# Kernel tuning notes

Measured on AMD Instinct MI355X. Metric: run time of the kernel, lower is better.

The kernel has to match this reference:

```python
import jax, jax.numpy as jnp
import numpy as np

N, E, C, H = 100000, 1600000, 64, 8
D = C // H  # head_dim = 8
LN_EPS = 1e-5


def _layer_norm(x, g, b):
    m = jnp.mean(x, axis=-1, keepdims=True)
    v = jnp.mean((x - m) ** 2, axis=-1, keepdims=True)
    return (x - m) * jax.lax.rsqrt(v + LN_EPS) * g + b


def setup_inputs() -> dict:
    key = jax.random.key(0)
    ks = jax.random.split(key, 20)
    s = 1.0 / np.sqrt(C)

    def lin(k, din, dout):
        return jax.random.uniform(k, (din, dout), jnp.float32, -1.0, 1.0) / np.sqrt(din)

    inp = {
        "node_states": jax.random.normal(ks[0], (N, C), jnp.float32),
        "edge_states": jax.random.normal(ks[1], (E, C), jnp.float32),
        "edge_index": jax.random.randint(ks[2], (2, E), 0, N),
        # attention projections
        "wq": lin(ks[3], C, C), "bq": jnp.zeros((C,), jnp.float32),
        "wk": lin(ks[4], C, C), "bk": jnp.zeros((C,), jnp.float32),
        "wv": lin(ks[5], C, C), "bv": jnp.zeros((C,), jnp.float32),
        "we": lin(ks[6], C, C), "be": jnp.zeros((C,), jnp.float32),
        "wno": lin(ks[7], C, C), "bno": jnp.zeros((C,), jnp.float32),
        "weo": lin(ks[8], H, C), "beo": jnp.zeros((C,), jnp.float32),
        # layer norms
        "n1g": jnp.ones((C,), jnp.float32), "n1b": jnp.zeros((C,), jnp.float32),
        "e1g": jnp.ones((C,), jnp.float32), "e1b": jnp.zeros((C,), jnp.float32),
        "n2g": jnp.ones((C,), jnp.float32), "n2b": jnp.zeros((C,), jnp.float32),
        "e2g": jnp.ones((C,), jnp.float32), "e2b": jnp.zeros((C,), jnp.float32),
        # node FFN
        "nf1w": lin(ks[9], C, 2 * C), "nf1b": jnp.zeros((2 * C,), jnp.float32),
        "nf2w": lin(ks[10], 2 * C, C), "nf2b": jnp.zeros((C,), jnp.float32),
        # edge FFN
        "ef1w": lin(ks[11], C, 2 * C), "ef1b": jnp.zeros((2 * C,), jnp.float32),
        "ef2w": lin(ks[12], 2 * C, C), "ef2b": jnp.zeros((C,), jnp.float32),
    }
    return inp


def reference(node_states, edge_states, wq, bq, wk, bk, wv, bv, we, be,
              wno, bno, weo, beo, n1g, n1b, e1g, e1b, n2g, n2b, e2g, e2b,
              nf1w, nf1b, nf2w, nf2b, ef1w, ef1b, ef2w, ef2b, edge_index):
    n = node_states.shape[0]
    e = edge_states.shape[0]
    src, dst = edge_index[0], edge_index[1]

    # pre-norm inputs
    ni = _layer_norm(node_states, n1g, n1b)
    ei = _layer_norm(edge_states, e1g, e1b)

    # projections -> [N,H,D] / [E,H,D]
    q = (ni @ wq + bq).reshape(n, H, D)
    k = (ni @ wk + bk).reshape(n, H, D)
    v = (ni @ wv + bv).reshape(n, H, D)
    edge_heads = ei.reshape(e, H, D)
    edge_score_heads = (ei @ we + be).reshape(e, H, D)

    # per-edge scores [E,H]
    scores = ((q[src] * k[dst]).sum(-1) + (edge_score_heads * edge_heads).sum(-1)) / np.sqrt(D)

    # segment softmax over edges sharing the same source node (per head)
    seg_max = jax.ops.segment_max(scores, src, num_segments=n)
    exp_s = jnp.exp(scores - seg_max[src])
    denom = jax.ops.segment_sum(exp_s, src, num_segments=n)
    attention = exp_s / (denom[src] + 1e-12)  # [E,H]

    # weighted scatter-add aggregation
    neighbor_state = ni[dst].reshape(e, H, D)
    weighted = attention[:, :, None] * (v[dst] * neighbor_state)  # [E,H,D]
    aggregated = jax.ops.segment_sum(weighted, src, num_segments=n).reshape(n, C)

    node_update = aggregated @ wno + bno
    edge_update = attention @ weo + beo

    node_s = node_states + node_update
    edge_s = edge_states + edge_update

    # FFN blocks with pre-norm residuals
    node_s = node_s + (jax.nn.relu(_layer_norm(node_s, n2g, n2b) @ nf1w + nf1b) @ nf2w + nf2b)
    edge_s = edge_s + (jax.nn.relu(_layer_norm(edge_s, e2g, e2b) @ ef1w + ef1b) @ ef2w + ef2b)
    return node_s, edge_s, attention
```

## Files before the change

### kernel.cpp

```cpp
#include <hip/hip_runtime.h>
#include <math.h>

#define NN 100000
#define EE 1600000

__device__ __forceinline__ float wsum64(float x){
  #pragma unroll
  for (int o = 32; o; o >>= 1) x += __shfl_xor(x, o, 64);
  return x;
}

__global__ __launch_bounds__(256) void k_node_pre(
    const float* __restrict__ ns,
    const float* __restrict__ wq, const float* __restrict__ bq,
    const float* __restrict__ wk, const float* __restrict__ bk,
    const float* __restrict__ wv, const float* __restrict__ bv,
    const float* __restrict__ n1g, const float* __restrict__ n1b,
    float* __restrict__ ni, float* __restrict__ q,
    float* __restrict__ k, float* __restrict__ v)
{
  __shared__ float swq[4096], swk[4096], swv[4096];
  for (int i = threadIdx.x; i < 4096; i += 256){ swq[i]=wq[i]; swk[i]=wk[i]; swv[i]=wv[i]; }
  __syncthreads();
  const int wave = threadIdx.x >> 6, lane = threadIdx.x & 63;
  const float gq = bq[lane], gk = bk[lane], gv = bv[lane];
  const float g1 = n1g[lane], b1 = n1b[lane];
  for (int n = blockIdx.x*4 + wave; n < NN; n += gridDim.x*4){
    const float x = ns[(size_t)n*64 + lane];
    const float m = wsum64(x) * (1.f/64.f);
    const float d = x - m;
    const float var = wsum64(d*d) * (1.f/64.f);
    const float niv = d * rsqrtf(var + 1e-5f) * g1 + b1;
    ni[(size_t)n*64 + lane] = niv;
    float aq = gq, ak = gk, av = gv;
    #pragma unroll
    for (int i = 0; i < 64; i++){
      const float e_ = __shfl(niv, i, 64);
      aq = fmaf(e_, swq[i*64 + lane], aq);
      ak = fmaf(e_, swk[i*64 + lane], ak);
      av = fmaf(e_, swv[i*64 + lane], av);
    }
    q[(size_t)n*64 + lane] = aq;
    k[(size_t)n*64 + lane] = ak;
    v[(size_t)n*64 + lane] = av;
  }
}

__global__ __launch_bounds__(256) void k_edge1(
    const float* __restrict__ es_in, const int* __restrict__ eidx,
    const float* __restrict__ we, const float* __restrict__ be,
    const float* __restrict__ e1g, const float* __restrict__ e1b,
    const float* __restrict__ q, const float* __restrict__ k,
    float* __restrict__ expo, float* __restrict__ denom)
{
  __shared__ float swe[4096];
  for (int i = threadIdx.x; i < 4096; i += 256) swe[i] = we[i];
  __syncthreads();
  const int wave = threadIdx.x >> 6, lane = threadIdx.x & 63;
  const float gbe = be[lane], g1 = e1g[lane], b1 = e1b[lane];
  for (size_t e = (size_t)blockIdx.x*4 + wave; e < EE; e += (size_t)gridDim.x*4){
    const float x = es_in[e*64 + lane];
    const float m = wsum64(x) * (1.f/64.f);
    const float d = x - m;
    const float var = wsum64(d*d) * (1.f/64.f);
    const float ei = d * rsqrtf(var + 1e-5f) * g1 + b1;
    float es = gbe;
    #pragma unroll
    for (int i = 0; i < 64; i++){
      es = fmaf(__shfl(ei, i, 64), swe[i*64 + lane], es);
    }
    const int src = eidx[e], dst = eidx[(size_t)EE + e];
    const float qs = q[(size_t)src*64 + lane];
    const float kd = k[(size_t)dst*64 + lane];
    float p = fmaf(qs, kd, es*ei);
    p += __shfl_xor(p, 1, 64); p += __shfl_xor(p, 2, 64); p += __shfl_xor(p, 4, 64);
    const float ev = __expf(p * 0.35355339059327373f);
    const float hv = __shfl(ev, (lane & 7)*8, 64);
    if (lane < 8){
      expo[e*8 + lane] = hv;
      atomicAdd(&denom[(size_t)src*8 + lane], hv);
    }
  }
}

__global__ __launch_bounds__(512) void k_edge2(
    const float* __restrict__ es_in, const int* __restrict__ eidx,
    const float* __restrict__ ni, const float* __restrict__ v,
    const float* __restrict__ weo, const float* __restrict__ beo,
    const float* __restrict__ e2g, const float* __restrict__ e2b,
    const float* __restrict__ ef1w, const float* __restrict__ ef1b,
    const float* __restrict__ ef2w, const float* __restrict__ ef2b,
    float* __restrict__ att, const float* __restrict__ denom,
    float* __restrict__ agg, float* __restrict__ eout)
{
  __shared__ float sf1[8192];
  __shared__ float sf2[8192];
  for (int i = threadIdx.x; i < 8192; i += 512){ sf1[i] = ef1w[i]; sf2[i] = ef2w[i]; }
  __syncthreads();
  const int wave = threadIdx.x >> 6, lane = threadIdx.x & 63;
  const int h = lane >> 3;
  float wo[8];
  #pragma unroll
  for (int hh = 0; hh < 8; hh++) wo[hh] = weo[hh*64 + lane];
  const float gbeo = beo[lane], g2 = e2g[lane], b2 = e2b[lane];
  const float gb1a = ef1b[lane], gb1b = ef1b[64 + lane], gb2 = ef2b[lane];

  for (size_t e = (size_t)blockIdx.x*8 + wave; e < EE; e += (size_t)gridDim.x*8){
    const int src = eidx[e], dst = eidx[(size_t)EE + e];
    const float ev  = att[e*8 + h];
    const float den = denom[(size_t)src*8 + h];
    const float a   = ev / (den + 1e-12f);
    const float av_ = __shfl(a, (lane & 7)*8, 64);
    if (lane < 8) att[e*8 + lane] = av_;

    const float vd = v[(size_t)dst*64 + lane];
    const float nd = ni[(size_t)dst*64 + lane];
    atomicAdd(&agg[(size_t)src*64 + lane], a*vd*nd);

    float eu = gbeo;
    #pragma unroll
    for (int hh = 0; hh < 8; hh++)
      eu = fmaf(__shfl(a, hh*8, 64), wo[hh], eu);
    const float esv = es_in[e*64 + lane] + eu;

    const float m = wsum64(esv) * (1.f/64.f);
    const float d = esv - m;
    const float var = wsum64(d*d) * (1.f/64.f);
    const float t = d * rsqrtf(var + 1e-5f) * g2 + b2;

    float h1a = gb1a, h1b = gb1b;
    #pragma unroll
    for (int i = 0; i < 64; i++){
      const float ti = __shfl(t, i, 64);
      h1a = fmaf(ti, sf1[i*128 + lane],      h1a);
      h1b = fmaf(ti, sf1[i*128 + 64 + lane], h1b);
    }
    h1a = fmaxf(h1a, 0.f); h1b = fmaxf(h1b, 0.f);
    float o = gb2;
    #pragma unroll
    for (int j = 0; j < 64; j++){
      o = fmaf(__shfl(h1a, j, 64), sf2[j*64 + lane],        o);
      o = fmaf(__shfl(h1b, j, 64), sf2[(64 + j)*64 + lane], o);
    }
    eout[e*64 + lane] = esv + o;
  }
}

__global__ __launch_bounds__(256) void k_node2(
    const float* __restrict__ ns, const float* __restrict__ agg,
    const float* __restrict__ wno, const float* __restrict__ bno,
    float* __restrict__ nout)
{
  __shared__ float sw[4096];
  for (int i = threadIdx.x; i < 4096; i += 256) sw[i] = wno[i];
  __syncthreads();
  const int wave = threadIdx.x >> 6, lane = threadIdx.x & 63;
  const float gb = bno[lane];
  for (int n = blockIdx.x*4 + wave; n < NN; n += gridDim.x*4){
    const float ag = agg[(size_t)n*64 + lane];
    float acc = gb;
    #pragma unroll
    for (int i = 0; i < 64; i++)
      acc = fmaf(__shfl(ag, i, 64), sw[i*64 + lane], acc);
    nout[(size_t)n*64 + lane] = ns[(size_t)n*64 + lane] + acc;
  }
}

__global__ __launch_bounds__(256) void k_node_ffn(
    float* __restrict__ x_inout,
    const float* __restrict__ g, const float* __restrict__ b,
    const float* __restrict__ f1w, const float* __restrict__ f1b,
    const float* __restrict__ f2w, const float* __restrict__ f2b)
{
  __shared__ float sf1[8192], sf2[8192];
  for (int i = threadIdx.x; i < 8192; i += 256){ sf1[i] = f1w[i]; sf2[i] = f2w[i]; }
  __syncthreads();
  const int wave = threadIdx.x >> 6, lane = threadIdx.x & 63;
  const float gg = g[lane], gb = b[lane];
  const float b1a = f1b[lane], b1b = f1b[64 + lane], bb2 = f2b[lane];
  for (int n = blockIdx.x*4 + wave; n < NN; n += gridDim.x*4){
    const float x = x_inout[(size_t)n*64 + lane];
    const float m = wsum64(x) * (1.f/64.f);
    const float d = x - m;
    const float var = wsum64(d*d) * (1.f/64.f);
    const float t = d * rsqrtf(var + 1e-5f) * gg + gb;
    float h1a = b1a, h1b = b1b;
    #pragma unroll
    for (int i = 0; i < 64; i++){
      const float ti = __shfl(t, i, 64);
      h1a = fmaf(ti, sf1[i*128 + lane],      h1a);
      h1b = fmaf(ti, sf1[i*128 + 64 + lane], h1b);
    }
    h1a = fmaxf(h1a, 0.f); h1b = fmaxf(h1b, 0.f);
    float o = bb2;
    #pragma unroll
    for (int j = 0; j < 64; j++){
      o = fmaf(__shfl(h1a, j, 64), sf2[j*64 + lane],        o);
      o = fmaf(__shfl(h1b, j, 64), sf2[(64 + j)*64 + lane], o);
    }
    x_inout[(size_t)n*64 + lane] = x + o;
  }
}

extern "C" void kernel_launch(void* const* d_in, const int* in_sizes, int n_in,
                              void* d_out, int out_size, void* d_ws, size_t ws_size,
                              hipStream_t stream)
{
  const float* node_states = (const float*)d_in[0];
  const float* edge_states = (const float*)d_in[1];
  const int*   eidx        = (const int*)  d_in[2];
  const float* wq  = (const float*)d_in[3];  const float* bq  = (const float*)d_in[4];
  const float* wk  = (const float*)d_in[5];  const float* bk  = (const float*)d_in[6];
  const float* wv  = (const float*)d_in[7];  const float* bv  = (const float*)d_in[8];
  const float* we  = (const float*)d_in[9];  const float* be  = (const float*)d_in[10];
  const float* wno = (const float*)d_in[11]; const float* bno = (const float*)d_in[12];
  const float* weo = (const float*)d_in[13]; const float* beo = (const float*)d_in[14];
  const float* n1g = (const float*)d_in[15]; const float* n1b = (const float*)d_in[16];
  const float* e1g = (const float*)d_in[17]; const float* e1b = (const float*)d_in[18];
  const float* n2g = (const float*)d_in[19]; const float* n2b = (const float*)d_in[20];
  const float* e2g = (const float*)d_in[21]; const float* e2b = (const float*)d_in[22];
  const float* nf1w= (const float*)d_in[23]; const float* nf1b= (const float*)d_in[24];
  const float* nf2w= (const float*)d_in[25]; const float* nf2b= (const float*)d_in[26];
  const float* ef1w= (const float*)d_in[27]; const float* ef1b= (const float*)d_in[28];
  const float* ef2w= (const float*)d_in[29]; const float* ef2b= (const float*)d_in[30];

  float* out      = (float*)d_out;
  float* out_node = out;
  float* out_edge = out + (size_t)NN*64;
  float* out_att  = out + (size_t)NN*64 + (size_t)EE*64;

  float* ws    = (float*)d_ws;
  float* w_ni  = ws;
  float* w_q   = ws + (size_t)NN*64;
  float* w_k   = ws + (size_t)NN*64*2;
  float* w_v   = ws + (size_t)NN*64*3;
  float* w_agg = ws + (size_t)NN*64*4;
  float* w_den = ws + (size_t)NN*64*5;

  hipMemsetAsync(w_agg, 0, (size_t)(NN*64 + NN*8)*sizeof(float), stream);

  hipLaunchKernelGGL(k_node_pre, dim3(6144), dim3(256), 0, stream,
      node_states, wq, bq, wk, bk, wv, bv, n1g, n1b, w_ni, w_q, w_k, w_v);
  hipLaunchKernelGGL(k_edge1, dim3(8192), dim3(256), 0, stream,
      edge_states, eidx, we, be, e1g, e1b, w_q, w_k, out_att, w_den);
  hipLaunchKernelGGL(k_edge2, dim3(4096), dim3(512), 0, stream,
      edge_states, eidx, w_ni, w_v, weo, beo, e2g, e2b,
      ef1w, ef1b, ef2w, ef2b, out_att, w_den, w_agg, out_edge);
  hipLaunchKernelGGL(k_node2, dim3(2048), dim3(256), 0, stream,
      node_states, w_agg, wno, bno, out_node);
  hipLaunchKernelGGL(k_node_ffn, dim3(2048), dim3(256), 0, stream,
      out_node, n2g, n2b, nf1w, nf1b, nf2w, nf2b);
}
```

Measured before the change: 18.11 ms.

## Build CSR by source node and replace atomic aggregation with per-node gather

Builds a CSR index of edges grouped by source node on every call (degree count, two-level scan, scatter). A new per-node kernel uses it to gather exp scores and v*ni products, computing the softmax denominator and aggregated messages without float atomics, and fuses the output projection into that kernel. v and ni are premultiplied in the node pre-pass so only one node array is gathered. The cost is several extra small kernels and an atomic-based CSR build each call, plus irregular per-node loops whose length depends on degree.

```diff
diff --git a/kernel.cpp b/kernel.cpp
--- a/kernel.cpp
+++ b/kernel.cpp
@@ -3,6 +3,9 @@
 
 #define NN 100000
 #define EE 1600000
+
+#define SCAN_BS 512
+#define NBLK ((NN + SCAN_BS - 1) / SCAN_BS)
 
 __device__ __forceinline__ float wsum64(float x){
   #pragma unroll
@@ -16,8 +19,7 @@
     const float* __restrict__ wk, const float* __restrict__ bk,
     const float* __restrict__ wv, const float* __restrict__ bv,
     const float* __restrict__ n1g, const float* __restrict__ n1b,
-    float* __restrict__ ni, float* __restrict__ q,
-    float* __restrict__ k, float* __restrict__ v)
+    float* __restrict__ q, float* __restrict__ k, float* __restrict__ vni)
 {
   __shared__ float swq[4096], swk[4096], swv[4096];
   for (int i = threadIdx.x; i < 4096; i += 256){ swq[i]=wq[i]; swk[i]=wk[i]; swv[i]=wv[i]; }
@@ -31,7 +33,6 @@
     const float d = x - m;
     const float var = wsum64(d*d) * (1.f/64.f);
     const float niv = d * rsqrtf(var + 1e-5f) * g1 + b1;
-    ni[(size_t)n*64 + lane] = niv;
     float aq = gq, ak = gk, av = gv;
     #pragma unroll
     for (int i = 0; i < 64; i++){
@@ -40,9 +41,78 @@
       ak = fmaf(e_, swk[i*64 + lane], ak);
       av = fmaf(e_, swv[i*64 + lane], av);
     }
-    q[(size_t)n*64 + lane] = aq;
-    k[(size_t)n*64 + lane] = ak;
-    v[(size_t)n*64 + lane] = av;
+    q[(size_t)n*64 + lane]   = aq;
+    k[(size_t)n*64 + lane]   = ak;
+    vni[(size_t)n*64 + lane] = av * niv;
+  }
+}
+
+__global__ __launch_bounds__(256) void k_deg(const int* __restrict__ eidx,
+                                             int* __restrict__ deg)
+{
+  for (size_t e = (size_t)blockIdx.x*256 + threadIdx.x; e < EE;
+       e += (size_t)gridDim.x*256)
+    atomicAdd(&deg[eidx[e]], 1);
+}
+
+__global__ __launch_bounds__(SCAN_BS) void k_blocksum(const int* __restrict__ deg,
+                                                      int* __restrict__ bsum)
+{
+  __shared__ int sd[SCAN_BS];
+  const int i = blockIdx.x*SCAN_BS + threadIdx.x;
+  sd[threadIdx.x] = (i < NN) ? deg[i] : 0;
+  __syncthreads();
+  for (int s = SCAN_BS/2; s; s >>= 1){
+    if (threadIdx.x < s) sd[threadIdx.x] += sd[threadIdx.x + s];
+    __syncthreads();
+  }
+  if (threadIdx.x == 0) bsum[blockIdx.x] = sd[0];
+}
+
+__global__ __launch_bounds__(256) void k_scan_bsum(const int* __restrict__ bsum,
+                                                   int* __restrict__ boff)
+{
+  __shared__ int s[256];
+  const int v = (threadIdx.x < NBLK) ? bsum[threadIdx.x] : 0;
+  s[threadIdx.x] = v;
+  __syncthreads();
+  for (int d = 1; d < 256; d <<= 1){
+    const int t = (threadIdx.x >= d) ? s[threadIdx.x - d] : 0;
+    __syncthreads();
+    s[threadIdx.x] += t;
+    __syncthreads();
+  }
+  if (threadIdx.x < NBLK) boff[threadIdx.x] = s[threadIdx.x] - v;
+}
+
+__global__ __launch_bounds__(SCAN_BS) void k_rowstart(const int* __restrict__ deg,
+                                                      const int* __restrict__ boff,
+                                                      int* __restrict__ rs)
+{
+  __shared__ int s[SCAN_BS];
+  const int i = blockIdx.x*SCAN_BS + threadIdx.x;
+  const int v = (i < NN) ? deg[i] : 0;
+  s[threadIdx.x] = v;
+  __syncthreads();
+  for (int d = 1; d < SCAN_BS; d <<= 1){
+    const int t = (threadIdx.x >= d) ? s[threadIdx.x - d] : 0;
+    __syncthreads();
+    s[threadIdx.x] += t;
+    __syncthreads();
+  }
+  if (i < NN) rs[i] = boff[blockIdx.x] + s[threadIdx.x] - v;
+}
+
+__global__ __launch_bounds__(256) void k_scatter(const int* __restrict__ eidx,
+                                                 const int* __restrict__ rs,
+                                                 int* __restrict__ cur,
+                                                 int* __restrict__ csr)
+{
+  for (size_t e = (size_t)blockIdx.x*256 + threadIdx.x; e < EE;
+       e += (size_t)gridDim.x*256){
+    const int s = eidx[e];
+    const int p = atomicAdd(&cur[s], 1);
+    csr[rs[s] + p] = (int)e;
   }
 }
 
@@ -51,7 +121,7 @@
     const float* __restrict__ we, const float* __restrict__ be,
     const float* __restrict__ e1g, const float* __restrict__ e1b,
     const float* __restrict__ q, const float* __restrict__ k,
-    float* __restrict__ expo, float* __restrict__ denom)
+    float* __restrict__ expo)
 {
   __shared__ float swe[4096];
   for (int i = threadIdx.x; i < 4096; i += 256) swe[i] = we[i];
@@ -76,22 +146,63 @@
     p += __shfl_xor(p, 1, 64); p += __shfl_xor(p, 2, 64); p += __shfl_xor(p, 4, 64);
     const float ev = __expf(p * 0.35355339059327373f);
     const float hv = __shfl(ev, (lane & 7)*8, 64);
-    if (lane < 8){
-      expo[e*8 + lane] = hv;
-      atomicAdd(&denom[(size_t)src*8 + lane], hv);
-    }
+    if (lane < 8) expo[e*8 + lane] = hv;
+  }
+}
+
+__global__ __launch_bounds__(256) void k_node_agg(
+    const float* __restrict__ ns, const int* __restrict__ eidx,
+    const float* __restrict__ vni, const float* __restrict__ expo,
+    float* __restrict__ den_out,
+    const int* __restrict__ row_start, const int* __restrict__ deg,
+    const int* __restrict__ csr,
+    const float* __restrict__ wno, const float* __restrict__ bno,
+    float* __restrict__ nout)
+{
+  __shared__ float sw[4096];
+  for (int i = threadIdx.x; i < 4096; i += 256) sw[i] = wno[i];
+  __syncthreads();
+  const int wave = threadIdx.x >> 6, lane = threadIdx.x & 63;
+  const int h = lane >> 3;
+  const float gb = bno[lane];
+  for (int n = blockIdx.x*4 + wave; n < NN; n += gridDim.x*4){
+    const int rs = row_start[n], dg = deg[n];
+    float den = 0.f, accU = 0.f;
+    for (int j0 = 0; j0 < dg; j0 += 64){
+      const int rem = dg - j0;
+      int eL = 0, dL = 0;
+      if (lane < rem){
+        eL = csr[rs + j0 + lane];
+        dL = eidx[(size_t)EE + eL];
+      }
+      const int cnt = rem < 64 ? rem : 64;
+      for (int j = 0; j < cnt; j++){
+        const int e   = __shfl(eL, j, 64);
+        const int dst = __shfl(dL, j, 64);
+        const float ev = expo[(size_t)e*8 + h];
+        den += ev;
+        accU = fmaf(ev, vni[(size_t)dst*64 + lane], accU);
+      }
+    }
+    const float denw = __shfl(den, (lane & 7)*8, 64);
+    if (lane < 8) den_out[(size_t)n*8 + lane] = denw;
+    const float acc = accU / (den + 1e-12f);
+    float o = gb;
+    #pragma unroll
+    for (int i = 0; i < 64; i++)
+      o = fmaf(__shfl(acc, i, 64), sw[i*64 + lane], o);
+    nout[(size_t)n*64 + lane] = ns[(size_t)n*64 + lane] + o;
   }
 }
 
 __global__ __launch_bounds__(512) void k_edge2(
     const float* __restrict__ es_in, const int* __restrict__ eidx,
-    const float* __restrict__ ni, const float* __restrict__ v,
     const float* __restrict__ weo, const float* __restrict__ beo,
     const float* __restrict__ e2g, const float* __restrict__ e2b,
     const float* __restrict__ ef1w, const float* __restrict__ ef1b,
     const float* __restrict__ ef2w, const float* __restrict__ ef2b,
-    float* __restrict__ att, const float* __restrict__ denom,
-    float* __restrict__ agg, float* __restrict__ eout)
+    float* __restrict__ att, const float* __restrict__ den,
+    float* __restrict__ eout)
 {
   __shared__ float sf1[8192];
   __shared__ float sf2[8192];
@@ -106,16 +217,12 @@
   const float gb1a = ef1b[lane], gb1b = ef1b[64 + lane], gb2 = ef2b[lane];
 
   for (size_t e = (size_t)blockIdx.x*8 + wave; e < EE; e += (size_t)gridDim.x*8){
-    const int src = eidx[e], dst = eidx[(size_t)EE + e];
-    const float ev  = att[e*8 + h];
-    const float den = denom[(size_t)src*8 + h];
-    const float a   = ev / (den + 1e-12f);
+    const int src = eidx[e];
+    const float ev = att[e*8 + h];
+    const float dn = den[(size_t)src*8 + h];
+    const float a  = ev / (dn + 1e-12f);
     const float av_ = __shfl(a, (lane & 7)*8, 64);
     if (lane < 8) att[e*8 + lane] = av_;
-
-    const float vd = v[(size_t)dst*64 + lane];
-    const float nd = ni[(size_t)dst*64 + lane];
-    atomicAdd(&agg[(size_t)src*64 + lane], a*vd*nd);
 
     float eu = gbeo;
     #pragma unroll
@@ -143,26 +250,6 @@
       o = fmaf(__shfl(h1b, j, 64), sf2[(64 + j)*64 + lane], o);
     }
     eout[e*64 + lane] = esv + o;
-  }
-}
-
-__global__ __launch_bounds__(256) void k_node2(
-    const float* __restrict__ ns, const float* __restrict__ agg,
-    const float* __restrict__ wno, const float* __restrict__ bno,
-    float* __restrict__ nout)
-{
-  __shared__ float sw[4096];
-  for (int i = threadIdx.x; i < 4096; i += 256) sw[i] = wno[i];
-  __syncthreads();
-  const int wave = threadIdx.x >> 6, lane = threadIdx.x & 63;
-  const float gb = bno[lane];
-  for (int n = blockIdx.x*4 + wave; n < NN; n += gridDim.x*4){
-    const float ag = agg[(size_t)n*64 + lane];
-    float acc = gb;
-    #pragma unroll
-    for (int i = 0; i < 64; i++)
-      acc = fmaf(__shfl(ag, i, 64), sw[i*64 + lane], acc);
-    nout[(size_t)n*64 + lane] = ns[(size_t)n*64 + lane] + acc;
   }
 }
 
@@ -230,24 +317,39 @@
   float* out_att  = out + (size_t)NN*64 + (size_t)EE*64;
 
   float* ws    = (float*)d_ws;
-  float* w_ni  = ws;
-  float* w_q   = ws + (size_t)NN*64;
-  float* w_k   = ws + (size_t)NN*64*2;
-  float* w_v   = ws + (size_t)NN*64*3;
-  float* w_agg = ws + (size_t)NN*64*4;
-  float* w_den = ws + (size_t)NN*64*5;
-
-  hipMemsetAsync(w_agg, 0, (size_t)(NN*64 + NN*8)*sizeof(float), stream);
+  float* w_q   = ws;
+  float* w_k   = ws + (size_t)NN*64;
+  float* w_vni = ws + (size_t)NN*64*2;
+  float* w_den = ws + (size_t)NN*64*3;
+  int*   w_deg  = (int*)(ws + (size_t)NN*64*3 + (size_t)NN*8);
+  int*   w_cur  = w_deg + NN;
+  int*   w_rs   = w_deg + 2*(size_t)NN;
+  int*   w_bsum = w_deg + 3*(size_t)NN;
+  int*   w_boff = w_bsum + NBLK;
+  int*   w_csr  = w_boff + NBLK;
+
+  hipMemsetAsync(w_deg, 0, 2*(size_t)NN*sizeof(int), stream);
 
   hipLaunchKernelGGL(k_node_pre, dim3(6144), dim3(256), 0, stream,
-      node_states, wq, bq, wk, bk, wv, bv, n1g, n1b, w_ni, w_q, w_k, w_v);
+      node_states, wq, bq, wk, bk, wv, bv, n1g, n1b, w_q, w_k, w_vni);
+
+  hipLaunchKernelGGL(k_deg,      dim3(1024), dim3(256),     0, stream, eidx, w_deg);
+  hipLaunchKernelGGL(k_blocksum, dim3(NBLK), dim3(SCAN_BS), 0, stream, w_deg, w_bsum);
+  hipLaunchKernelGGL(k_scan_bsum,dim3(1),    dim3(256),     0, stream, w_bsum, w_boff);
+  hipLaunchKernelGGL(k_rowstart, dim3(NBLK), dim3(SCAN_BS), 0, stream, w_deg, w_boff, w_rs);
+  hipLaunchKernelGGL(k_scatter,  dim3(1024), dim3(256),     0, stream, eidx, w_rs, w_cur, w_csr);
+
   hipLaunchKernelGGL(k_edge1, dim3(8192), dim3(256), 0, stream,
-      edge_states, eidx, we, be, e1g, e1b, w_q, w_k, out_att, w_den);
+      edge_states, eidx, we, be, e1g, e1b, w_q, w_k, out_att);
+
+  hipLaunchKernelGGL(k_node_agg, dim3(6144), dim3(256), 0, stream,
+      node_states, eidx, w_vni, out_att, w_den, w_rs, w_deg, w_csr,
+      wno, bno, out_node);
+
   hipLaunchKernelGGL(k_edge2, dim3(4096), dim3(512), 0, stream,
-      edge_states, eidx, w_ni, w_v, weo, beo, e2g, e2b,
-      ef1w, ef1b, ef2w, ef2b, out_att, w_den, w_agg, out_edge);
-  hipLaunchKernelGGL(k_node2, dim3(2048), dim3(256), 0, stream,
-      node_states, w_agg, wno, bno, out_node);
+      edge_states, eidx, weo, beo, e2g, e2b,
+      ef1w, ef1b, ef2w, ef2b, out_att, w_den, out_edge);
+
   hipLaunchKernelGGL(k_node_ffn, dim3(2048), dim3(256), 0, stream,
       out_node, n2g, n2b, nf1w, nf1b, nf2w, nf2b);
 }
```

Measured after the change: 17.77 ms. Within noise of the previous version (-1.8%).
